# Performance work log

Hardware: AMD Instinct MI355X
Metric: run time of the kernel (lower is better)

## Reference

```python
import jax, jax.numpy as jnp
import numpy as np


def setup_inputs() -> dict:
    key = jax.random.key(0)
    k1, k2, k3 = jax.random.split(key, 3)
    B, S, H = 16, 4096, 512           # batch, frames, encoder feature dim
    G, V, D = 2, 320, 128             # groups, codevectors/group, group dim
    return {
        "hidden_states": jax.random.normal(k1, (B, S, H), dtype=jnp.float32),
        "W_proj": jax.random.normal(k2, (H, G * D), dtype=jnp.float32) * 0.02,
        "b_proj": jnp.zeros((G * D,), dtype=jnp.float32),
        "codevectors": jax.random.normal(k3, (G, V, D), dtype=jnp.float32),
    }


def reference(hidden_states, W_proj, b_proj, codevectors):
    B, S, _ = hidden_states.shape
    G, V, D = codevectors.shape
    # project to codevector_dim, split into groups: [B,S,G,D]
    h = (hidden_states @ W_proj + b_proj).reshape(B, S, G, D)
    # squared L2 distances per group, via ||h||^2 - 2 h.c + ||c||^2 -> [G,B,S,V]
    hc = jnp.einsum('bsgd,gvd->gbsv', h, codevectors)
    h2 = jnp.sum(h * h, axis=-1).transpose(2, 0, 1)[..., None]      # [G,B,S,1]
    c2 = jnp.sum(codevectors * codevectors, axis=-1)[:, None, None, :]  # [G,1,1,V]
    distances = h2 - 2.0 * hc + c2                                   # [G,B,S,V]
    indices = jnp.argmin(distances, axis=-1)                         # [G,B,S]
    encodings = jax.nn.one_hot(indices, V, dtype=jnp.float32)        # [G,B,S,V]
    # one-hot matmul gather of selected codevectors, concat groups -> [B,S,G*D]
    quantized_features = jnp.einsum('gbsv,gvd->bsgd', encodings, codevectors).reshape(B, S, G * D)
    # codebook usage perplexity
    avg_probs = jnp.clip(jnp.mean(encodings, axis=(1, 2)), 1e-10, 1.0)  # [G,V]
    perplexity = jnp.mean(jnp.exp(-jnp.sum(avg_probs * jnp.log(avg_probs + 1e-10), axis=-1)))
    return quantized_features, encodings, distances, perplexity
```

## Files before the change

kernel.cpp:

```cpp
#include <hip/hip_runtime.h>
#include <cfloat>

#define M_TOTAL 65536
#define K_H     512
#define GD      256
#define NG      2
#define ND      128
#define NV      320

#define Q_OFF     0
#define ENC_OFF   16777216
#define DIST_OFF  58720256
#define PERP_OFF  100663296

__global__ void c2_kernel(const float* __restrict__ C, float* __restrict__ c2out) {
  int gv = blockIdx.x * 64 + threadIdx.x;
  const float4* p = (const float4*)(C + (size_t)gv * ND);
  float s = 0.f;
#pragma unroll 8
  for (int q = 0; q < 32; ++q) {
    float4 v = p[q];
    s += v.x * v.x + v.y * v.y + v.z * v.z + v.w * v.w;
  }
  c2out[gv] = s;
}

__global__ __launch_bounds__(256, 2) void quant_main(
    const float* __restrict__ X,
    const float* __restrict__ W,
    const float* __restrict__ bias,
    const float* __restrict__ C,
    const float* __restrict__ c2,
    int* __restrict__ hist,
    float* __restrict__ out) {
  __shared__ float hs[64 * 128];
  __shared__ float reg2[8192];

  const int t   = threadIdx.x;
  const int tx  = t & 15;
  const int ty  = t >> 4;
  const int row0 = blockIdx.x * 64;

  float* out_q    = out + Q_OFF;
  float* out_enc  = out + ENC_OFF;
  float* out_dist = out + DIST_OFF;

  for (int g = 0; g < NG; ++g) {
    float acc1[4][8];
#pragma unroll
    for (int i = 0; i < 4; ++i)
#pragma unroll
      for (int j = 0; j < 8; ++j) acc1[i][j] = 0.f;

    for (int kc = 0; kc < 32; ++kc) {
      __syncthreads();
      {
        int r = t >> 2, kq = t & 3;
        float4 x4 = *(const float4*)(X + (size_t)(row0 + r) * K_H + kc * 16 + kq * 4);
        reg2[68 * (4 * kq + 0) + r] = x4.x;
        reg2[68 * (4 * kq + 1) + r] = x4.y;
        reg2[68 * (4 * kq + 2) + r] = x4.z;
        reg2[68 * (4 * kq + 3) + r] = x4.w;
      }
#pragma unroll
      for (int i = 0; i < 2; ++i) {
        int fq = t + 256 * i;
        int k = fq >> 5, c4 = fq & 31;
        float4 w4 = *(const float4*)(W + (size_t)(kc * 16 + k) * GD + g * ND + 4 * c4);
        int c = 4 * c4;
        *(float4*)&reg2[1088 + 160 * k + 20 * (c >> 4) + (c & 15)] = w4;
      }
      __syncthreads();
#pragma unroll
      for (int k = 0; k < 16; ++k) {
        float4 a = *(const float4*)&reg2[68 * k + 4 * ty];
        int wb = 1088 + 160 * k + 20 * (tx >> 1) + 8 * (tx & 1);
        float4 w0 = *(const float4*)&reg2[wb];
        float4 w1 = *(const float4*)&reg2[wb + 4];
        float av[4] = {a.x, a.y, a.z, a.w};
        float wv[8] = {w0.x, w0.y, w0.z, w0.w, w1.x, w1.y, w1.z, w1.w};
#pragma unroll
        for (int i = 0; i < 4; ++i)
#pragma unroll
          for (int j = 0; j < 8; ++j) acc1[i][j] += av[i] * wv[j];
      }
    }
#pragma unroll
    for (int j = 0; j < 8; ++j) {
      float bj = bias[g * ND + 8 * tx + j];
#pragma unroll
      for (int i = 0; i < 4; ++i) acc1[i][j] += bj;
    }
#pragma unroll
    for (int i = 0; i < 4; ++i) {
      int r = 4 * ty + i, sw = r & 7;
      float4 v0 = make_float4(acc1[i][0], acc1[i][1], acc1[i][2], acc1[i][3]);
      float4 v1 = make_float4(acc1[i][4], acc1[i][5], acc1[i][6], acc1[i][7]);
      *(float4*)&hs[128 * r + 4 * ((2 * tx) ^ sw)]     = v0;
      *(float4*)&hs[128 * r + 4 * ((2 * tx + 1) ^ sw)] = v1;
    }
    __syncthreads();

    float h2r[4];
#pragma unroll
    for (int i = 0; i < 4; ++i) {
      int r = 4 * ty + i, sw = r & 7;
      float s = 0.f;
#pragma unroll
      for (int qq = 0; qq < 2; ++qq) {
        int q = tx + 16 * qq;
        float4 v = *(const float4*)&hs[128 * r + 4 * (q ^ sw)];
        s += v.x * v.x + v.y * v.y + v.z * v.z + v.w * v.w;
      }
#pragma unroll
      for (int off = 1; off < 16; off <<= 1) s += __shfl_xor(s, off);
      h2r[i] = s;
    }

    float runval[4]; int runidx[4];
#pragma unroll
    for (int i = 0; i < 4; ++i) { runval[i] = FLT_MAX; runidx[i] = 0; }

    for (int vc = 0; vc < 5; ++vc) {
      int vbase = vc * 64;
      __syncthreads();
#pragma unroll
      for (int i = 0; i < 8; ++i) {
        int fq = t + 256 * i;
        int v = fq >> 5, q = fq & 31;
        float4 cv = *(const float4*)(C + (size_t)((g * NV + vbase + v) * ND) + 4 * q);
        *(float4*)&reg2[128 * v + 4 * (q ^ (v & 7))] = cv;
      }
      __syncthreads();
      float acc[4][4];
#pragma unroll
      for (int i = 0; i < 4; ++i)
#pragma unroll
        for (int j = 0; j < 4; ++j) acc[i][j] = 0.f;
#pragma unroll 4
      for (int q = 0; q < 32; ++q) {
        float4 a[4], b[4];
#pragma unroll
        for (int i = 0; i < 4; ++i) {
          int r = 4 * ty + i;
          a[i] = *(const float4*)&hs[128 * r + 4 * (q ^ (r & 7))];
        }
#pragma unroll
        for (int j = 0; j < 4; ++j) {
          int v = tx + 16 * j;
          b[j] = *(const float4*)&reg2[128 * v + 4 * (q ^ (v & 7))];
        }
#pragma unroll
        for (int i = 0; i < 4; ++i)
#pragma unroll
          for (int j = 0; j < 4; ++j)
            acc[i][j] += a[i].x * b[j].x + a[i].y * b[j].y +
                         a[i].z * b[j].z + a[i].w * b[j].w;
      }
      float c2v[4];
#pragma unroll
      for (int j = 0; j < 4; ++j) c2v[j] = c2[g * NV + vbase + tx + 16 * j];
#pragma unroll
      for (int i = 0; i < 4; ++i) {
        int rg = row0 + 4 * ty + i;
        size_t dbase = (size_t)(g * M_TOTAL + rg) * NV + vbase;
#pragma unroll
        for (int j = 0; j < 4; ++j) {
          float d = h2r[i] - 2.f * acc[i][j] + c2v[j];
          out_dist[dbase + tx + 16 * j] = d;
          int vidx = vbase + tx + 16 * j;
          if (d < runval[i]) { runval[i] = d; runidx[i] = vidx; }
        }
      }
    }

    int fidx[4];
#pragma unroll
    for (int i = 0; i < 4; ++i) {
      float v = runval[i]; int idx = runidx[i];
#pragma unroll
      for (int off = 1; off < 16; off <<= 1) {
        float ov = __shfl_xor(v, off);
        int oi = __shfl_xor(idx, off);
        if (ov < v || (ov == v && oi < idx)) { v = ov; idx = oi; }
      }
      fidx[i] = idx;
      if (tx == 0) {
        int rg = row0 + 4 * ty + i;
        out_enc[(size_t)(g * M_TOTAL + rg) * NV + idx] = 1.0f;
        atomicAdd(&hist[g * NV + idx], 1);
      }
    }
    __syncthreads();
    if (tx == 0) {
#pragma unroll
      for (int i = 0; i < 4; ++i) ((int*)reg2)[4 * ty + i] = fidx[i];
    }
    __syncthreads();
#pragma unroll
    for (int it = 0; it < 8; ++it) {
      int flat = t + 256 * it;
      int r = flat >> 5, q = flat & 31;
      int idx = ((int*)reg2)[r];
      float4 cv = *(const float4*)(C + (size_t)((g * NV + idx) * ND) + 4 * q);
      *(float4*)(out_q + (size_t)(row0 + r) * GD + g * ND + 4 * q) = cv;
    }
  }
}

__global__ void perp_kernel(const int* __restrict__ hist, float* __restrict__ outp) {
  int t = threadIdx.x;
  float s0 = 0.f, s1 = 0.f;
  for (int v = t; v < NV; v += 64) {
    float p0 = fminf(fmaxf((float)hist[v] * (1.0f / 65536.f), 1e-10f), 1.0f);
    float p1 = fminf(fmaxf((float)hist[NV + v] * (1.0f / 65536.f), 1e-10f), 1.0f);
    s0 += p0 * logf(p0 + 1e-10f);
    s1 += p1 * logf(p1 + 1e-10f);
  }
#pragma unroll
  for (int off = 1; off < 64; off <<= 1) {
    s0 += __shfl_xor(s0, off);
    s1 += __shfl_xor(s1, off);
  }
  if (t == 0) outp[0] = 0.5f * (expf(-s0) + expf(-s1));
}

extern "C" void kernel_launch(void* const* d_in, const int* in_sizes, int n_in,
                              void* d_out, int out_size, void* d_ws, size_t ws_size,
                              hipStream_t stream) {
  const float* X    = (const float*)d_in[0];
  const float* W    = (const float*)d_in[1];
  const float* bias = (const float*)d_in[2];
  const float* C    = (const float*)d_in[3];
  float* out = (float*)d_out;

  int*   hist = (int*)d_ws;
  float* c2   = (float*)d_ws + 1024;

  hipMemsetAsync(out + ENC_OFF, 0, (size_t)41943040 * 4, stream);
  hipMemsetAsync(d_ws, 0, 4096, stream);

  c2_kernel<<<10, 64, 0, stream>>>(C, c2);
  quant_main<<<1024, 256, 0, stream>>>(X, W, bias, C, c2, hist, out);
  perp_kernel<<<1, 64, 0, stream>>>(hist, out + PERP_OFF);
}
```

Baseline: 1.144 ms.

## Stream codebook from global, write full one-hot rows, drop encoding memset

Drops the separate memset of the encodings buffer; the kernel now writes each full one-hot row with vector nontemporal stores. Distance stores also become nontemporal. The codebook tile is no longer staged in shared memory: each thread reads codevectors straight from global/L2 in 80-wide chunks, which shrinks shared memory so launch bounds can request 4 blocks per CU. The projection K-tile is halved to fit the smaller staging buffer. This trades extra global/L2 reads of the codebook and more K-loop iterations for higher occupancy and one less full pass over the large encodings output.

```diff
diff --git a/kernel.cpp b/kernel.cpp
--- a/kernel.cpp
+++ b/kernel.cpp
@@ -12,6 +12,8 @@
 #define ENC_OFF   16777216
 #define DIST_OFF  58720256
 #define PERP_OFF  100663296
+
+typedef float f4v __attribute__((ext_vector_type(4)));
 
 __global__ void c2_kernel(const float* __restrict__ C, float* __restrict__ c2out) {
   int gv = blockIdx.x * 64 + threadIdx.x;
@@ -25,7 +27,7 @@
   c2out[gv] = s;
 }
 
-__global__ __launch_bounds__(256, 2) void quant_main(
+__global__ __launch_bounds__(256, 4) void quant_main(
     const float* __restrict__ X,
     const float* __restrict__ W,
     const float* __restrict__ bias,
@@ -34,7 +36,7 @@
     int* __restrict__ hist,
     float* __restrict__ out) {
   __shared__ float hs[64 * 128];
-  __shared__ float reg2[8192];
+  __shared__ float reg2[1824];
 
   const int t   = threadIdx.x;
   const int tx  = t & 15;
@@ -52,29 +54,24 @@
 #pragma unroll
       for (int j = 0; j < 8; ++j) acc1[i][j] = 0.f;
 
-    for (int kc = 0; kc < 32; ++kc) {
+    for (int kc = 0; kc < 64; ++kc) {
       __syncthreads();
       {
         int r = t >> 2, kq = t & 3;
-        float4 x4 = *(const float4*)(X + (size_t)(row0 + r) * K_H + kc * 16 + kq * 4);
-        reg2[68 * (4 * kq + 0) + r] = x4.x;
-        reg2[68 * (4 * kq + 1) + r] = x4.y;
-        reg2[68 * (4 * kq + 2) + r] = x4.z;
-        reg2[68 * (4 * kq + 3) + r] = x4.w;
-      }
-#pragma unroll
-      for (int i = 0; i < 2; ++i) {
-        int fq = t + 256 * i;
-        int k = fq >> 5, c4 = fq & 31;
-        float4 w4 = *(const float4*)(W + (size_t)(kc * 16 + k) * GD + g * ND + 4 * c4);
-        int c = 4 * c4;
-        *(float4*)&reg2[1088 + 160 * k + 20 * (c >> 4) + (c & 15)] = w4;
+        float2 x2 = *(const float2*)(X + (size_t)(row0 + r) * K_H + kc * 8 + 2 * kq);
+        reg2[68 * (2 * kq + 0) + r] = x2.x;
+        reg2[68 * (2 * kq + 1) + r] = x2.y;
+      }
+      {
+        int k = t >> 5, c4 = t & 31;
+        float4 w4 = *(const float4*)(W + (size_t)(kc * 8 + k) * GD + g * ND + 4 * c4);
+        *(float4*)&reg2[544 + 160 * k + 20 * (c4 >> 2) + 4 * (c4 & 3)] = w4;
       }
       __syncthreads();
 #pragma unroll
-      for (int k = 0; k < 16; ++k) {
+      for (int k = 0; k < 8; ++k) {
         float4 a = *(const float4*)&reg2[68 * k + 4 * ty];
-        int wb = 1088 + 160 * k + 20 * (tx >> 1) + 8 * (tx & 1);
+        int wb = 544 + 160 * k + 20 * (tx >> 1) + 8 * (tx & 1);
         float4 w0 = *(const float4*)&reg2[wb];
         float4 w1 = *(const float4*)&reg2[wb + 4];
         float av[4] = {a.x, a.y, a.z, a.w};
@@ -121,54 +118,43 @@
 #pragma unroll
     for (int i = 0; i < 4; ++i) { runval[i] = FLT_MAX; runidx[i] = 0; }
 
-    for (int vc = 0; vc < 5; ++vc) {
-      int vbase = vc * 64;
-      __syncthreads();
-#pragma unroll
-      for (int i = 0; i < 8; ++i) {
-        int fq = t + 256 * i;
-        int v = fq >> 5, q = fq & 31;
-        float4 cv = *(const float4*)(C + (size_t)((g * NV + vbase + v) * ND) + 4 * q);
-        *(float4*)&reg2[128 * v + 4 * (q ^ (v & 7))] = cv;
-      }
-      __syncthreads();
-      float acc[4][4];
+    for (int vc = 0; vc < 4; ++vc) {
+      int vb = 80 * vc;
+      float acc[4][5];
 #pragma unroll
       for (int i = 0; i < 4; ++i)
 #pragma unroll
-        for (int j = 0; j < 4; ++j) acc[i][j] = 0.f;
+        for (int j = 0; j < 5; ++j) acc[i][j] = 0.f;
+      const float* Cg = C + (size_t)(g * NV + vb + tx) * ND;
 #pragma unroll 4
       for (int q = 0; q < 32; ++q) {
-        float4 a[4], b[4];
+        float4 a[4];
 #pragma unroll
         for (int i = 0; i < 4; ++i) {
           int r = 4 * ty + i;
           a[i] = *(const float4*)&hs[128 * r + 4 * (q ^ (r & 7))];
         }
 #pragma unroll
-        for (int j = 0; j < 4; ++j) {
-          int v = tx + 16 * j;
-          b[j] = *(const float4*)&reg2[128 * v + 4 * (q ^ (v & 7))];
+        for (int j = 0; j < 5; ++j) {
+          float4 b = *(const float4*)(Cg + (size_t)(2048 * j) + 4 * q);
+#pragma unroll
+          for (int i = 0; i < 4; ++i)
+            acc[i][j] += a[i].x * b.x + a[i].y * b.y +
+                         a[i].z * b.z + a[i].w * b.w;
         }
-#pragma unroll
-        for (int i = 0; i < 4; ++i)
-#pragma unroll
-          for (int j = 0; j < 4; ++j)
-            acc[i][j] += a[i].x * b[j].x + a[i].y * b[j].y +
-                         a[i].z * b[j].z + a[i].w * b[j].w;
-      }
-      float c2v[4];
-#pragma unroll
-      for (int j = 0; j < 4; ++j) c2v[j] = c2[g * NV + vbase + tx + 16 * j];
+      }
+      float c2v[5];
+#pragma unroll
+      for (int j = 0; j < 5; ++j) c2v[j] = c2[g * NV + vb + tx + 16 * j];
 #pragma unroll
       for (int i = 0; i < 4; ++i) {
         int rg = row0 + 4 * ty + i;
-        size_t dbase = (size_t)(g * M_TOTAL + rg) * NV + vbase;
-#pragma unroll
-        for (int j = 0; j < 4; ++j) {
+        size_t dbase = (size_t)(g * M_TOTAL + rg) * NV + vb;
+#pragma unroll
+        for (int j = 0; j < 5; ++j) {
           float d = h2r[i] - 2.f * acc[i][j] + c2v[j];
-          out_dist[dbase + tx + 16 * j] = d;
-          int vidx = vbase + tx + 16 * j;
+          __builtin_nontemporal_store(d, out_dist + dbase + tx + 16 * j);
+          int vidx = vb + tx + 16 * j;
           if (d < runval[i]) { runval[i] = d; runidx[i] = vidx; }
         }
       }
@@ -185,13 +171,26 @@
         if (ov < v || (ov == v && oi < idx)) { v = ov; idx = oi; }
       }
       fidx[i] = idx;
-      if (tx == 0) {
-        int rg = row0 + 4 * ty + i;
-        out_enc[(size_t)(g * M_TOTAL + rg) * NV + idx] = 1.0f;
-        atomicAdd(&hist[g * NV + idx], 1);
-      }
-    }
-    __syncthreads();
+      if (tx == 0) atomicAdd(&hist[g * NV + idx], 1);
+    }
+
+#pragma unroll
+    for (int i = 0; i < 4; ++i) {
+      int rg = row0 + 4 * ty + i;
+      float* rowp = out_enc + (size_t)(g * M_TOTAL + rg) * NV;
+      int fi = fidx[i];
+#pragma unroll
+      for (int jj = 0; jj < 5; ++jj) {
+        int q = tx + 16 * jj;
+        f4v e;
+        e.x = (fi == 4 * q + 0) ? 1.f : 0.f;
+        e.y = (fi == 4 * q + 1) ? 1.f : 0.f;
+        e.z = (fi == 4 * q + 2) ? 1.f : 0.f;
+        e.w = (fi == 4 * q + 3) ? 1.f : 0.f;
+        __builtin_nontemporal_store(e, (f4v*)(rowp + 4 * q));
+      }
+    }
+
     if (tx == 0) {
 #pragma unroll
       for (int i = 0; i < 4; ++i) ((int*)reg2)[4 * ty + i] = fidx[i];
@@ -237,7 +236,6 @@
   int*   hist = (int*)d_ws;
   float* c2   = (float*)d_ws + 1024;
 
-  hipMemsetAsync(out + ENC_OFF, 0, (size_t)41943040 * 4, stream);
   hipMemsetAsync(d_ws, 0, 4096, stream);
 
   c2_kernel<<<10, 64, 0, stream>>>(C, c2);
```

After: 2.034 ms. 77.8% more time.
